# Optimization experiments

Hardware: AMD Instinct MI355X
Metric: run time of the kernel (lower is better)

Reference implementation:

```python
import jax, jax.numpy as jnp
from jax import lax
import numpy as np
from functools import partial

B, N, T, H, L = 16, 256, 4, 128, 2
VOCAB, OUT_VOCAB, MAX_STEPS = 1000, 1000, 15


def setup_inputs() -> dict:
    key = jax.random.key(0)
    ks = jax.random.split(key, 13)
    data = jax.random.randint(ks[0], (B, N, T), 0, VOCAB)
    true_branch_nodes = jax.random.randint(ks[1], (B, N), 0, N)
    false_branch_nodes = jax.random.randint(ks[2], (B, N), 0, N)
    exit_index = jax.random.randint(ks[3], (B,), 0, N)
    steps = jax.random.randint(ks[4], (B,), 1, MAX_STEPS + 1)
    s_in = 1.0 / np.sqrt(H)
    s_cat = 1.0 / np.sqrt(2 * L * H)
    embed = jax.random.uniform(ks[5], (VOCAB, H), jnp.float32, -0.1, 0.1)
    Wi = jax.random.normal(ks[6], (L, H, 4 * H), jnp.float32) * s_in
    Wh = jax.random.normal(ks[7], (L, H, 4 * H), jnp.float32) * s_in
    b_lstm = jnp.zeros((L, 4 * H), jnp.float32)
    Wb = jax.random.normal(ks[8], (2 * L * H, 2), jnp.float32) * s_cat
    bb = jax.random.normal(ks[9], (2,), jnp.float32) * 1e-6
    Wo = jax.random.normal(ks[10], (2 * L * H, OUT_VOCAB), jnp.float32) * s_cat
    bo = jax.random.normal(ks[11], (OUT_VOCAB,), jnp.float32) * 1e-6
    return dict(data=data, true_branch_nodes=true_branch_nodes,
                false_branch_nodes=false_branch_nodes, exit_index=exit_index,
                steps=steps, embed=embed, Wi=Wi, Wh=Wh, b_lstm=b_lstm,
                Wb=Wb, bb=bb, Wo=Wo, bo=bo)


def _lstm_step(Wi_l, Wh_l, b_l, c, h, x):
    # flax LSTMCell math: gates from input (no bias) + recurrent (bias)
    z = x @ Wi_l + h @ Wh_l + b_l  # [..., 4H]
    i, f, g, o = jnp.split(z, 4, axis=-1)
    c2 = jax.nn.sigmoid(f) * c + jax.nn.sigmoid(i) * jnp.tanh(g)
    h2 = jax.nn.sigmoid(o) * jnp.tanh(c2)
    return c2, h2


def _forward(data, true_branch_nodes, false_branch_nodes, exit_index, steps,
             embed, Wi, Wh, b_lstm, Wb, bb, Wo, bo):
    emb = embed[data]                       # [B, N, T, H]
    cs = jnp.zeros((L, B, N, H), embed.dtype)
    hs = jnp.zeros((L, B, N, H), embed.dtype)
    ip = jnp.zeros((B, N), embed.dtype).at[:, 0].set(1.0)
    b_idx = jnp.arange(B)

    seg_b = jax.vmap(partial(jax.ops.segment_sum, num_segments=N))        # [B,N,...] , [B,N]
    seg_lb = jax.vmap(seg_b, in_axes=(0, None))                           # [L,B,N,H]

    def execute(cs, hs):
        # run the stacked LSTM over the T statement tokens at every node
        def tok_step(carry, x_t):
            cs, hs = carry
            inp = x_t
            nc, nh = [], []
            for l in range(L):
                c2, h2 = _lstm_step(Wi[l], Wh[l], b_lstm[l], cs[l], hs[l], inp)
                nc.append(c2); nh.append(h2)
                inp = h2
            return (jnp.stack(nc), jnp.stack(nh)), None
        (cs, hs), _ = lax.scan(tok_step, (cs, hs), jnp.moveaxis(emb, 2, 0))
        return cs, hs

    def step(carry, _):
        cs, hs, ip, idx = carry
        cs_c, hs_c = execute(cs, hs)
        # exit node keeps its previous hidden state
        cs_c = cs_c.at[:, b_idx, exit_index].set(cs[:, b_idx, exit_index])
        hs_c = hs_c.at[:, b_idx, exit_index].set(hs[:, b_idx, exit_index])
        # branch decision from concatenated (c, h) of every layer: [B, N, 2LH]
        feats = jnp.concatenate([x for l in range(L) for x in (cs_c[l], hs_c[l])], axis=-1)
        branch = jax.nn.softmax(feats @ Wb + bb, axis=-1)
        wt = branch[..., 0] * ip            # [B, N]
        wf = branch[..., 1] * ip
        ip_new = seg_b(wt, true_branch_nodes) + seg_b(wf, false_branch_nodes)
        denom = (ip_new + 1e-7)[None, :, :, None]
        def agg(h):
            return (seg_lb(h * wt[None, :, :, None], true_branch_nodes)
                    + seg_lb(h * wf[None, :, :, None], false_branch_nodes)) / denom
        cs_new, hs_new = agg(cs_c), agg(hs_c)
        live = idx < steps                   # [B]
        cs = jnp.where(live[None, :, None, None], cs_new, cs)
        hs = jnp.where(live[None, :, None, None], hs_new, hs)
        ip = jnp.where(live[:, None], ip_new, ip)
        return (cs, hs, ip, idx + 1), None

    (cs, hs, ip, _), _ = lax.scan(step, (cs, hs, ip, jnp.zeros((), jnp.int32)),
                                  None, length=MAX_STEPS)
    fc = cs[:, b_idx, exit_index]           # [L, B, H]
    fh = hs[:, b_idx, exit_index]
    final = jnp.concatenate([x for l in range(L) for x in (fc[l], fh[l])], axis=-1)
    logits = final @ Wo + bo                # [B, OUT_VOCAB]
    return logits[:, None, :]


def reference(data, true_branch_nodes, false_branch_nodes, exit_index, steps,
              embed, Wi, Wh, b_lstm, Wb, bb, Wo, bo):
    return _forward(data, true_branch_nodes, false_branch_nodes, exit_index,
                    steps, embed, Wi, Wh, b_lstm, Wb, bb, Wo, bo)
```

## Files before the change

kernel.cpp:

```cpp
#include <hip/hip_runtime.h>
#include <hip/hip_bf16.h>
#include <stdint.h>
#include <stddef.h>

static constexpr int BB = 16, NN = 256, TT = 4, HH = 128;
static constexpr int MM = BB * NN;
static constexpr int CC = 512;
static constexpr int OUTV = 1000;
static constexpr int MAXS = 15;
static constexpr int SP = 132;

typedef float f32x4 __attribute__((ext_vector_type(4)));
typedef short s16x8 __attribute__((ext_vector_type(8)));

__device__ __forceinline__ float sigf(float x) { return 1.0f / (1.0f + __expf(-x)); }
__device__ __forceinline__ float tanhr(float x) { return 2.0f / (1.0f + __expf(-2.0f * x)) - 1.0f; }
__device__ __forceinline__ unsigned short f2bu(float a) {
  return __builtin_bit_cast(unsigned short, __float2bfloat16(a));
}


__global__ void init_kernel(float* __restrict__ S, float* __restrict__ ip, int* __restrict__ count) {
  int tid = blockIdx.x * blockDim.x + threadIdx.x;
  int stride = gridDim.x * blockDim.x;
  int total = 4 * MM * HH;
  for (int i = tid; i < total; i += stride) S[i] = 0.0f;
  for (int i = tid; i < MM; i += stride) {
    ip[i] = ((i & (NN - 1)) == 0) ? 1.0f : 0.0f;
    count[i] = 0;
  }
}

__global__ void swz_kernel(const float* __restrict__ W, unsigned short* __restrict__ out) {
  int i = blockIdx.x * 256 + threadIdx.x;
  int j = i & 7, ln = (i >> 3) & 63, kb = (i >> 9) & 3, ct = i >> 11;
  int n = ln & 15, q = ln >> 4;
  int k = kb * 32 + q * 8 + j;
  int col = ct * 16 + n;
  out[i] = f2bu(W[k * CC + col]);
}

__global__ void xw0tab_kernel(const float* __restrict__ embed, const float* __restrict__ Wi0,
                              const float* __restrict__ b0, float* __restrict__ tab) {
  const int v0 = blockIdx.x * 8;
  const int j = threadIdx.x;
  __shared__ float A[8][HH];
  for (int s = j; s < 8 * HH; s += 256) {
    int r = s >> 7, k = s & 127;
    int v = v0 + r; if (v >= OUTV) v = OUTV - 1;
    A[r][k] = embed[(size_t)v * HH + k];
  }
  __syncthreads();
  float za[8], zb[8];
  {
    float ba = b0[j], bbv = b0[j + 256];
#pragma unroll
    for (int r = 0; r < 8; ++r) { za[r] = ba; zb[r] = bbv; }
  }
#pragma unroll 4
  for (int k = 0; k < HH; ++k) {
    float wa = Wi0[k * CC + j], wb = Wi0[k * CC + j + 256];
#pragma unroll
    for (int r = 0; r < 8; ++r) { za[r] += A[r][k] * wa; zb[r] += A[r][k] * wb; }
  }
#pragma unroll
  for (int r = 0; r < 8; ++r) {
    tab[(size_t)(v0 + r) * CC + j] = za[r];
    tab[(size_t)(v0 + r) * CC + j + 256] = zb[r];
  }
}

__global__ void edge_count(const int* __restrict__ tb, const int* __restrict__ fb,
                           int* __restrict__ count) {
  int e = blockIdx.x * blockDim.x + threadIdx.x;
  if (e >= 2 * MM) return;
  int b = e >> 9, r = e & 511, n = r >> 1, bit = r & 1;
  int tgt = bit ? fb[b * NN + n] : tb[b * NN + n];
  atomicAdd(&count[b * NN + tgt], 1);
}

__global__ void edge_scan(int* __restrict__ count, int* __restrict__ offs) {
  int b = blockIdx.x, tid = threadIdx.x;
  __shared__ int s[256];
  int v = count[b * NN + tid];
  s[tid] = v;
  __syncthreads();
  for (int off = 1; off < 256; off <<= 1) {
    int t = (tid >= off) ? s[tid - off] : 0;
    __syncthreads();
    s[tid] += t;
    __syncthreads();
  }
  offs[b * NN + tid] = b * 2 * NN + s[tid] - v;
  count[b * NN + tid] = 0;
  if (b == 0 && tid == 0) offs[MM] = 2 * MM;
}

__global__ void edge_fill(const int* __restrict__ tb, const int* __restrict__ fb,
                          const int* __restrict__ offs, int* __restrict__ cursor,
                          int* __restrict__ edges) {
  int e = blockIdx.x * blockDim.x + threadIdx.x;
  if (e >= 2 * MM) return;
  int b = e >> 9, r = e & 511, n = r >> 1, bit = r & 1;
  int tgt = bit ? fb[b * NN + n] : tb[b * NN + n];
  int pos = offs[b * NN + tgt] + atomicAdd(&cursor[b * NN + tgt], 1);
  edges[pos] = (n << 1) | bit;
}


__global__ __launch_bounds__(512, 2) void step_kernel(
    float* __restrict__ Sc0g, float* __restrict__ Sh0g,
    float* __restrict__ Sc1g, float* __restrict__ Sh1g,
    const float* __restrict__ Wr0, const float* __restrict__ Wr1,
    const float* __restrict__ Wr2, const float* __restrict__ Wr3,
    float* __restrict__ Ww0, float* __restrict__ Ww1,
    float* __restrict__ Ww2, float* __restrict__ Ww3,
    const float* __restrict__ wtR, const float* __restrict__ wfR,
    float* __restrict__ wtW, float* __restrict__ wfW,
    const float* __restrict__ ipg,
    const int* __restrict__ offs, const int* __restrict__ edges,
    const float* __restrict__ tab,
    const unsigned short* __restrict__ swzWh0, const unsigned short* __restrict__ swzWi1,
    const unsigned short* __restrict__ swzWh1, const float* __restrict__ b1,
    const float* __restrict__ Wb, const float* __restrict__ bb,
    const int* __restrict__ data, const int* __restrict__ exi,
    const int* __restrict__ steps, int step) {
  const int row0 = blockIdx.x * 16;
  const int b = row0 >> 8;
  const int sb = steps[b];
  const bool aggLive = (step >= 1) && ((step - 1) < sb);
  const bool lstmLive = (step < sb);
  if (!aggLive && !lstmLive) return;

  const int tid = threadIdx.x;
  const int w = tid >> 6;
  const int lane = tid & 63;
  const int n16 = lane & 15, qq = lane >> 4;
  const int kcol = w * 16 + n16;

  __shared__ float c0L[16 * SP], h0L[16 * SP], c1L[16 * SP], h1L[16 * SP];
  __shared__ __align__(16) unsigned short hA0[2048], hA1[2048];
  __shared__ float exitP[4][HH];
  __shared__ float ipL[16];
  __shared__ int toks[64];

  if (aggLive) {
    const int l = tid & 31;
    const int m = tid >> 5;
    const int node = row0 + m;
    int beg = offs[node], end = offs[node + 1];
    float a0x = 0.f, a0y = 0.f, a0z = 0.f, a0w = 0.f;
    float a1x = 0.f, a1y = 0.f, a1z = 0.f, a1w = 0.f;
    float a2x = 0.f, a2y = 0.f, a2z = 0.f, a2w = 0.f;
    float a3x = 0.f, a3y = 0.f, a3z = 0.f, a3w = 0.f;
    float wsum = 0.f;
    for (int e = beg; e < end; ++e) {
      int rec = edges[e];
      int src = (b << 8) + (rec >> 1);
      float wv = (rec & 1) ? wfR[src] : wtR[src];
      wsum += wv;
      float4 x0 = ((const float4*)Wr0)[src * 32 + l];
      float4 x1 = ((const float4*)Wr1)[src * 32 + l];
      float4 x2 = ((const float4*)Wr2)[src * 32 + l];
      float4 x3 = ((const float4*)Wr3)[src * 32 + l];
      a0x += wv * x0.x; a0y += wv * x0.y; a0z += wv * x0.z; a0w += wv * x0.w;
      a1x += wv * x1.x; a1y += wv * x1.y; a1z += wv * x1.z; a1w += wv * x1.w;
      a2x += wv * x2.x; a2y += wv * x2.y; a2z += wv * x2.z; a2w += wv * x2.w;
      a3x += wv * x3.x; a3y += wv * x3.y; a3z += wv * x3.z; a3w += wv * x3.w;
    }
    float inv = 1.0f / (wsum + 1e-7f);
    float4 o0 = { a0x * inv, a0y * inv, a0z * inv, a0w * inv };
    float4 o1 = { a1x * inv, a1y * inv, a1z * inv, a1w * inv };
    float4 o2 = { a2x * inv, a2y * inv, a2z * inv, a2w * inv };
    float4 o3 = { a3x * inv, a3y * inv, a3z * inv, a3w * inv };
    ((float4*)c0L)[m * (SP / 4) + l] = o0;
    ((float4*)h0L)[m * (SP / 4) + l] = o1;
    ((float4*)c1L)[m * (SP / 4) + l] = o2;
    ((float4*)h1L)[m * (SP / 4) + l] = o3;
    if (l == 0) ipL[m] = wsum;
    if (!lstmLive) {
      ((float4*)Sc0g)[node * 32 + l] = o0;
      ((float4*)Sh0g)[node * 32 + l] = o1;
      ((float4*)Sc1g)[node * 32 + l] = o2;
      ((float4*)Sh1g)[node * 32 + l] = o3;
    }
  } else {
    for (int s = tid; s < 16 * HH; s += 512) {
      int m = s >> 7, k = s & 127;
      size_t g = (size_t)(row0 + m) * HH + k;
      c0L[m * SP + k] = Sc0g[g];
      h0L[m * SP + k] = Sh0g[g];
      c1L[m * SP + k] = Sc1g[g];
      h1L[m * SP + k] = Sh1g[g];
    }
    if (tid < 16) ipL[tid] = ipg[row0 + tid];
  }
  if (!lstmLive) return;

  s16x8 B0[4][4], B1[4][4];
  const s16x8* pWh0 = (const s16x8*)swzWh0;
  const s16x8* pWh1 = (const s16x8*)swzWh1;
  const s16x8* pWi1 = (const s16x8*)swzWi1;
  float b1v[4];
#pragma unroll
  for (int g = 0; g < 4; ++g) {
    int ci = w + 8 * g;
#pragma unroll
    for (int kb = 0; kb < 4; ++kb) {
      B0[g][kb] = pWh0[(ci * 4 + kb) * 64 + lane];
      B1[g][kb] = pWh1[(ci * 4 + kb) * 64 + lane];
    }
    b1v[g] = b1[ci * 16 + n16];
  }

  const int exnode = exi[b];
  const int exm = exnode - (row0 & (NN - 1));
  if (tid < 64) toks[tid] = data[(row0 + (tid >> 2)) * TT + (tid & 3)];
  __syncthreads();

  if (exm >= 0 && exm < 16 && tid < 128) {
    exitP[0][tid] = c0L[exm * SP + tid];
    exitP[1][tid] = h0L[exm * SP + tid];
    exitP[2][tid] = c1L[exm * SP + tid];
    exitP[3][tid] = h1L[exm * SP + tid];
  }

  const int kb0 = kcol >> 5, q0 = (kcol >> 3) & 3, j0 = kcol & 7;
  const int basePos = (kb0 * 64 + q0 * 16) * 8 + j0;
  float c0r[4], c1r[4], h0r[4], h1r[4];
#pragma unroll
  for (int r = 0; r < 4; ++r) {
    int m = qq * 4 + r;
    c0r[r] = c0L[m * SP + kcol];
    c1r[r] = c1L[m * SP + kcol];
    h0r[r] = h0L[m * SP + kcol];
    h1r[r] = h1L[m * SP + kcol];
    hA0[basePos + m * 8] = f2bu(h0r[r]);
    hA1[basePos + m * 8] = f2bu(h1r[r]);
  }
  __syncthreads();

  const s16x8* hA0v = (const s16x8*)hA0;
  const s16x8* hA1v = (const s16x8*)hA1;

  for (int t = 0; t < TT; ++t) {
    s16x8 a0[4], a1b[4];
#pragma unroll
    for (int kb = 0; kb < 4; ++kb) { a0[kb] = hA0v[kb * 64 + lane]; a1b[kb] = hA1v[kb * 64 + lane]; }
    f32x4 d0[4];
#pragma unroll
    for (int g = 0; g < 4; ++g) {
      int colz = (w + 8 * g) * 16 + n16;
#pragma unroll
      for (int r = 0; r < 4; ++r)
        d0[g][r] = tab[(size_t)toks[(qq * 4 + r) * 4 + t] * CC + colz];
    }
    __syncthreads();

#pragma unroll
    for (int g = 0; g < 4; ++g)
#pragma unroll
      for (int kb = 0; kb < 4; ++kb)
        d0[g] = __builtin_amdgcn_mfma_f32_16x16x32_bf16(a0[kb], B0[g][kb], d0[g], 0, 0, 0);

#pragma unroll
    for (int r = 0; r < 4; ++r) {
      float cn = sigf(d0[1][r]) * c0r[r] + sigf(d0[0][r]) * tanhr(d0[2][r]);
      float hn = sigf(d0[3][r]) * tanhr(cn);
      c0r[r] = cn; h0r[r] = hn;
      hA0[basePos + (qq * 4 + r) * 8] = f2bu(hn);
    }
    __syncthreads();

    s16x8 a1a[4];
#pragma unroll
    for (int kb = 0; kb < 4; ++kb) a1a[kb] = hA0v[kb * 64 + lane];
    f32x4 d1[4];
#pragma unroll
    for (int g = 0; g < 4; ++g) {
      int ci = w + 8 * g;
      s16x8 wi[4];
#pragma unroll
      for (int kb = 0; kb < 4; ++kb) wi[kb] = pWi1[(ci * 4 + kb) * 64 + lane];
      f32x4 d = { b1v[g], b1v[g], b1v[g], b1v[g] };
#pragma unroll
      for (int kb = 0; kb < 4; ++kb)
        d = __builtin_amdgcn_mfma_f32_16x16x32_bf16(a1a[kb], wi[kb], d, 0, 0, 0);
#pragma unroll
      for (int kb = 0; kb < 4; ++kb)
        d = __builtin_amdgcn_mfma_f32_16x16x32_bf16(a1b[kb], B1[g][kb], d, 0, 0, 0);
      d1[g] = d;
    }

#pragma unroll
    for (int r = 0; r < 4; ++r) {
      float cn = sigf(d1[1][r]) * c1r[r] + sigf(d1[0][r]) * tanhr(d1[2][r]);
      float hn = sigf(d1[3][r]) * tanhr(cn);
      c1r[r] = cn; h1r[r] = hn;
      hA1[basePos + (qq * 4 + r) * 8] = f2bu(hn);
    }
    __syncthreads();
  }

#pragma unroll
  for (int r = 0; r < 4; ++r) {
    int m = qq * 4 + r;
    c0L[m * SP + kcol] = c0r[r];
    h0L[m * SP + kcol] = h0r[r];
    c1L[m * SP + kcol] = c1r[r];
    h1L[m * SP + kcol] = h1r[r];
  }
  __syncthreads();

  {
    const int m = tid >> 5, sub = tid & 31;
    const int row = row0 + m;
    const bool isExit = (m == exm);
    float z0 = 0.f, z1 = 0.f;
#pragma unroll
    for (int u = 0; u < 16; ++u) {
      int k = u * 32 + sub;
      int seg = k >> 7, kk = k & 127;
      float fk;
      if (isExit) {
        fk = exitP[seg][kk];
      } else {
        fk = (seg == 0) ? c0L[m * SP + kk] : (seg == 1) ? h0L[m * SP + kk]
           : (seg == 2) ? c1L[m * SP + kk] : h1L[m * SP + kk];
      }
      z0 += fk * Wb[2 * k];
      z1 += fk * Wb[2 * k + 1];
    }
#pragma unroll
    for (int off = 16; off >= 1; off >>= 1) {
      z0 += __shfl_xor(z0, off);
      z1 += __shfl_xor(z1, off);
    }
    if (sub == 0) {
      z0 += bb[0]; z1 += bb[1];
      float mx = fmaxf(z0, z1);
      float e0 = __expf(z0 - mx), e1 = __expf(z1 - mx);
      float inv = 1.0f / (e0 + e1);
      float ipv = ipL[m];
      wtW[row] = e0 * inv * ipv;
      wfW[row] = e1 * inv * ipv;
    }
  }

  for (int s = tid; s < 16 * HH; s += 512) {
    int m = s >> 7, k = s & 127;
    bool ex = (m == exm);
    size_t g = (size_t)(row0 + m) * HH + k;
    Ww0[g] = ex ? exitP[0][k] : c0L[m * SP + k];
    Ww1[g] = ex ? exitP[1][k] : h0L[m * SP + k];
    Ww2[g] = ex ? exitP[2][k] : c1L[m * SP + k];
    Ww3[g] = ex ? exitP[3][k] : h1L[m * SP + k];
  }
}

__global__ void final_kernel(const float* __restrict__ Sc0, const float* __restrict__ Sh0,
                             const float* __restrict__ Sc1, const float* __restrict__ Sh1,
                             const int* __restrict__ exi, const float* __restrict__ Wo,
                             const float* __restrict__ bo, float* __restrict__ out) {
  const int b = blockIdx.x >> 2;
  const int vt = blockIdx.x & 3;
  const int tid = threadIdx.x;
  __shared__ float f[512];
  int row = b * NN + exi[b];
  if (tid < 128) {
    size_t g = (size_t)row * HH + tid;
    f[tid] = Sc0[g];
    f[128 + tid] = Sh0[g];
    f[256 + tid] = Sc1[g];
    f[384 + tid] = Sh1[g];
  }
  __syncthreads();
  if (tid < 250) {
    int v = vt * 250 + tid;
    float acc = bo[v];
#pragma unroll 8
    for (int k = 0; k < 512; ++k) acc += f[k] * Wo[(size_t)k * OUTV + v];
    out[b * OUTV + v] = acc;
  }
}

__global__ void zero_out_kernel(float* __restrict__ out, int n) {
  int i = blockIdx.x * blockDim.x + threadIdx.x;
  if (i < n) out[i] = 0.0f;
}


extern "C" void kernel_launch(void* const* d_in, const int* in_sizes, int n_in,
                              void* d_out, int out_size, void* d_ws, size_t ws_size,
                              hipStream_t stream) {
  const int* data = (const int*)d_in[0];
  const int* tb   = (const int*)d_in[1];
  const int* fb   = (const int*)d_in[2];
  const int* exi  = (const int*)d_in[3];
  const int* steps = (const int*)d_in[4];
  const float* embed = (const float*)d_in[5];
  const float* Wi = (const float*)d_in[6];
  const float* Wh = (const float*)d_in[7];
  const float* bl = (const float*)d_in[8];
  const float* Wb = (const float*)d_in[9];
  const float* bb = (const float*)d_in[10];
  const float* Wo = (const float*)d_in[11];
  const float* bo = (const float*)d_in[12];
  float* out = (float*)d_out;

  const float* Wi0 = Wi;
  const float* Wi1 = Wi + HH * CC;
  const float* Wh0 = Wh;
  const float* Wh1 = Wh + HH * CC;
  const float* b0 = bl;
  const float* b1 = bl + CC;

  float* ws = (float*)d_ws;
  size_t off = 0;
  float* tab = ws + off;  off += (size_t)1024 * CC;
  float* Sc0 = ws + off;  off += (size_t)MM * HH;
  float* Sh0 = ws + off;  off += (size_t)MM * HH;
  float* Sc1 = ws + off;  off += (size_t)MM * HH;
  float* Sh1 = ws + off;  off += (size_t)MM * HH;
  float* WA[4], *WB[4];
  for (int i = 0; i < 4; ++i) { WA[i] = ws + off; off += (size_t)MM * HH; }
  for (int i = 0; i < 4; ++i) { WB[i] = ws + off; off += (size_t)MM * HH; }
  unsigned short* swzWh0 = (unsigned short*)(ws + off); off += (size_t)HH * CC / 2;
  unsigned short* swzWi1 = (unsigned short*)(ws + off); off += (size_t)HH * CC / 2;
  unsigned short* swzWh1 = (unsigned short*)(ws + off); off += (size_t)HH * CC / 2;
  float* ip = ws + off;   off += MM;
  float* wtA = ws + off;  off += MM;
  float* wfA = ws + off;  off += MM;
  float* wtB = ws + off;  off += MM;
  float* wfB = ws + off;  off += MM;
  int* count = (int*)(ws + off); off += MM;
  int* offs  = (int*)(ws + off); off += MM + 16;
  int* edges = (int*)(ws + off); off += 2 * MM;
  (void)in_sizes; (void)n_in; (void)out_size;

  if (ws_size < off * sizeof(float)) {
    zero_out_kernel<<<(BB * OUTV + 255) / 256, 256, 0, stream>>>(out, BB * OUTV);
    return;
  }

  init_kernel<<<256, 256, 0, stream>>>(Sc0, ip, count);
  swz_kernel<<<256, 256, 0, stream>>>(Wh0, swzWh0);
  swz_kernel<<<256, 256, 0, stream>>>(Wi1, swzWi1);
  swz_kernel<<<256, 256, 0, stream>>>(Wh1, swzWh1);
  xw0tab_kernel<<<128, 256, 0, stream>>>(embed, Wi0, b0, tab);
  edge_count<<<(2 * MM + 255) / 256, 256, 0, stream>>>(tb, fb, count);
  edge_scan<<<BB, 256, 0, stream>>>(count, offs);
  edge_fill<<<(2 * MM + 255) / 256, 256, 0, stream>>>(tb, fb, offs, count, edges);

  for (int s = 0; s <= MAXS; ++s) {
    float** Wwr = (s & 1) ? WB : WA;
    float** Wrd = (s & 1) ? WA : WB;
    float* wtWp = (s & 1) ? wtB : wtA;
    float* wfWp = (s & 1) ? wfB : wfA;
    float* wtRp = (s & 1) ? wtA : wtB;
    float* wfRp = (s & 1) ? wfA : wfB;
    step_kernel<<<MM / 16, 512, 0, stream>>>(
        Sc0, Sh0, Sc1, Sh1,
        Wrd[0], Wrd[1], Wrd[2], Wrd[3],
        Wwr[0], Wwr[1], Wwr[2], Wwr[3],
        wtRp, wfRp, wtWp, wfWp, ip,
        offs, edges, tab, swzWh0, swzWi1, swzWh1, b1, Wb, bb,
        data, exi, steps, s);
  }
  final_kernel<<<BB * 4, 256, 0, stream>>>(Sc0, Sh0, Sc1, Sh1, exi, Wo, bo, out);
}
```

Baseline: 596.4 us.

## Fuse all setup, step and final kernels into one cooperative persistent kernel

Replaces the roughly 25 separate launches (init, swizzle, table build, edge CSR build, 16 step launches and the final projection) with one cooperative kernel of 256 blocks, using grid.sync between phases and steps. Loop-invariant bf16 weight fragments are loaded into registers once instead of every step. The state-zeroing init kernel and the full state arrays are dropped: zero state is synthesized in LDS and only the exit-node row is saved for the final projection. The aim is to remove launch overhead and redundant global traffic, at the cost of depending on all blocks being co-resident and on the expense of grid-wide barriers.

```diff
diff --git a/kernel.cpp b/kernel.cpp
--- a/kernel.cpp
+++ b/kernel.cpp
@@ -1,7 +1,10 @@
 #include <hip/hip_runtime.h>
+#include <hip/hip_cooperative_groups.h>
 #include <hip/hip_bf16.h>
 #include <stdint.h>
 #include <stddef.h>
+
+namespace cg = cooperative_groups;
 
 static constexpr int BB = 16, NN = 256, TT = 4, HH = 128;
 static constexpr int MM = BB * NN;
@@ -9,6 +12,7 @@
 static constexpr int OUTV = 1000;
 static constexpr int MAXS = 15;
 static constexpr int SP = 132;
+static constexpr int SSZ = MM * HH;
 
 typedef float f32x4 __attribute__((ext_vector_type(4)));
 typedef short s16x8 __attribute__((ext_vector_type(8)));
@@ -19,368 +23,336 @@
   return __builtin_bit_cast(unsigned short, __float2bfloat16(a));
 }
 
-
-__global__ void init_kernel(float* __restrict__ S, float* __restrict__ ip, int* __restrict__ count) {
-  int tid = blockIdx.x * blockDim.x + threadIdx.x;
-  int stride = gridDim.x * blockDim.x;
-  int total = 4 * MM * HH;
-  for (int i = tid; i < total; i += stride) S[i] = 0.0f;
-  for (int i = tid; i < MM; i += stride) {
-    ip[i] = ((i & (NN - 1)) == 0) ? 1.0f : 0.0f;
-    count[i] = 0;
-  }
-}
-
-__global__ void swz_kernel(const float* __restrict__ W, unsigned short* __restrict__ out) {
-  int i = blockIdx.x * 256 + threadIdx.x;
-  int j = i & 7, ln = (i >> 3) & 63, kb = (i >> 9) & 3, ct = i >> 11;
-  int n = ln & 15, q = ln >> 4;
-  int k = kb * 32 + q * 8 + j;
-  int col = ct * 16 + n;
-  out[i] = f2bu(W[k * CC + col]);
-}
-
-__global__ void xw0tab_kernel(const float* __restrict__ embed, const float* __restrict__ Wi0,
-                              const float* __restrict__ b0, float* __restrict__ tab) {
-  const int v0 = blockIdx.x * 8;
-  const int j = threadIdx.x;
-  __shared__ float A[8][HH];
-  for (int s = j; s < 8 * HH; s += 256) {
-    int r = s >> 7, k = s & 127;
-    int v = v0 + r; if (v >= OUTV) v = OUTV - 1;
-    A[r][k] = embed[(size_t)v * HH + k];
-  }
-  __syncthreads();
-  float za[8], zb[8];
-  {
-    float ba = b0[j], bbv = b0[j + 256];
-#pragma unroll
-    for (int r = 0; r < 8; ++r) { za[r] = ba; zb[r] = bbv; }
-  }
+__global__ __launch_bounds__(512, 2) void mega_kernel(
+    const int* __restrict__ data, const int* __restrict__ tb, const int* __restrict__ fb,
+    const int* __restrict__ exi, const int* __restrict__ steps,
+    const float* __restrict__ embed, const float* __restrict__ Wi, const float* __restrict__ Wh,
+    const float* __restrict__ bl, const float* __restrict__ Wb, const float* __restrict__ bbp,
+    const float* __restrict__ Wo, const float* __restrict__ bo,
+    float* __restrict__ out, float* __restrict__ ws) {
+  cg::grid_group grid = cg::this_grid();
+  const int blk = blockIdx.x;
+  const int tid = threadIdx.x;
+
+  float* tab = ws;
+  float* WAb = ws + (size_t)1024 * CC;
+  float* WBb = WAb + 4 * (size_t)SSZ;
+  unsigned short* swz = (unsigned short*)(WBb + 4 * (size_t)SSZ);
+  float* wtwf = (float*)(swz + 3 * 65536);
+  int* offs = (int*)(wtwf + 4 * MM);
+  int* edges = offs + MM + 16;
+  float* fin = (float*)(edges + 2 * MM);
+
+  const float* Wi0 = Wi;
+  const float* Wi1 = Wi + HH * CC;
+  const float* Wh0 = Wh;
+  const float* Wh1 = Wh + HH * CC;
+  const float* b0 = bl;
+  const float* b1 = bl + CC;
+  unsigned short* swzWh0 = swz;
+  unsigned short* swzWi1 = swz + 65536;
+  unsigned short* swzWh1 = swz + 2 * 65536;
+  float* wtA = wtwf;          float* wfA = wtwf + MM;
+  float* wtB = wtwf + 2 * MM; float* wfB = wtwf + 3 * MM;
+
+  __shared__ float c0L[16 * SP], h0L[16 * SP], c1L[16 * SP], h1L[16 * SP];
+  __shared__ __align__(16) unsigned short hA0[2048], hA1[2048];
+  __shared__ float exitP[512];
+  __shared__ float ipL[16];
+  __shared__ int toks[64];
+
+  for (int i = blk * 512 + tid; i < 3 * 65536; i += 256 * 512) {
+    int mtx = i >> 16, ii = i & 65535;
+    const float* W = (mtx == 0) ? Wh0 : (mtx == 1) ? Wi1 : Wh1;
+    int j = ii & 7, ln = (ii >> 3) & 63, kb = (ii >> 9) & 3, ct = ii >> 11;
+    int n = ln & 15, q = ln >> 4;
+    swz[i] = f2bu(W[(kb * 32 + q * 8 + j) * CC + ct * 16 + n]);
+  }
+  if (blk < 16) {
+    int* cnt = (int*)h0L;
+    int* sc = cnt + 256;
+    int* cur = cnt + 512;
+    if (tid < 256) cnt[tid] = 0;
+    __syncthreads();
+    const int n = tid >> 1, bit = tid & 1;
+    const int tgt = bit ? fb[blk * NN + n] : tb[blk * NN + n];
+    atomicAdd(&cnt[tgt], 1);
+    __syncthreads();
+    if (tid < 256) sc[tid] = cnt[tid];
+    __syncthreads();
+    for (int ofs = 1; ofs < 256; ofs <<= 1) {
+      int t2 = (tid < 256 && tid >= ofs) ? sc[tid - ofs] : 0;
+      __syncthreads();
+      if (tid < 256) sc[tid] += t2;
+      __syncthreads();
+    }
+    if (tid < 256) { offs[blk * NN + tid] = blk * 2 * NN + sc[tid] - cnt[tid]; cur[tid] = 0; }
+    if (blk == 0 && tid == 0) offs[MM] = 2 * MM;
+    __syncthreads();
+    int lpos = sc[tgt] - cnt[tgt] + atomicAdd(&cur[tgt], 1);
+    edges[blk * 2 * NN + lpos] = (n << 1) | bit;
+  }
+  if (blk < 250) {
+    float* A = c0L;
+    const int v0 = blk * 4;
+    A[tid] = embed[(size_t)(v0 + (tid >> 7)) * HH + (tid & 127)];
+    __syncthreads();
+    const int j = tid;
+    float a0 = b0[j], a1 = a0, a2 = a0, a3 = a0;
 #pragma unroll 4
-  for (int k = 0; k < HH; ++k) {
-    float wa = Wi0[k * CC + j], wb = Wi0[k * CC + j + 256];
-#pragma unroll
-    for (int r = 0; r < 8; ++r) { za[r] += A[r][k] * wa; zb[r] += A[r][k] * wb; }
-  }
-#pragma unroll
-  for (int r = 0; r < 8; ++r) {
-    tab[(size_t)(v0 + r) * CC + j] = za[r];
-    tab[(size_t)(v0 + r) * CC + j + 256] = zb[r];
-  }
-}
-
-__global__ void edge_count(const int* __restrict__ tb, const int* __restrict__ fb,
-                           int* __restrict__ count) {
-  int e = blockIdx.x * blockDim.x + threadIdx.x;
-  if (e >= 2 * MM) return;
-  int b = e >> 9, r = e & 511, n = r >> 1, bit = r & 1;
-  int tgt = bit ? fb[b * NN + n] : tb[b * NN + n];
-  atomicAdd(&count[b * NN + tgt], 1);
-}
-
-__global__ void edge_scan(int* __restrict__ count, int* __restrict__ offs) {
-  int b = blockIdx.x, tid = threadIdx.x;
-  __shared__ int s[256];
-  int v = count[b * NN + tid];
-  s[tid] = v;
-  __syncthreads();
-  for (int off = 1; off < 256; off <<= 1) {
-    int t = (tid >= off) ? s[tid - off] : 0;
-    __syncthreads();
-    s[tid] += t;
-    __syncthreads();
-  }
-  offs[b * NN + tid] = b * 2 * NN + s[tid] - v;
-  count[b * NN + tid] = 0;
-  if (b == 0 && tid == 0) offs[MM] = 2 * MM;
-}
-
-__global__ void edge_fill(const int* __restrict__ tb, const int* __restrict__ fb,
-                          const int* __restrict__ offs, int* __restrict__ cursor,
-                          int* __restrict__ edges) {
-  int e = blockIdx.x * blockDim.x + threadIdx.x;
-  if (e >= 2 * MM) return;
-  int b = e >> 9, r = e & 511, n = r >> 1, bit = r & 1;
-  int tgt = bit ? fb[b * NN + n] : tb[b * NN + n];
-  int pos = offs[b * NN + tgt] + atomicAdd(&cursor[b * NN + tgt], 1);
-  edges[pos] = (n << 1) | bit;
-}
-
-
-__global__ __launch_bounds__(512, 2) void step_kernel(
-    float* __restrict__ Sc0g, float* __restrict__ Sh0g,
-    float* __restrict__ Sc1g, float* __restrict__ Sh1g,
-    const float* __restrict__ Wr0, const float* __restrict__ Wr1,
-    const float* __restrict__ Wr2, const float* __restrict__ Wr3,
-    float* __restrict__ Ww0, float* __restrict__ Ww1,
-    float* __restrict__ Ww2, float* __restrict__ Ww3,
-    const float* __restrict__ wtR, const float* __restrict__ wfR,
-    float* __restrict__ wtW, float* __restrict__ wfW,
-    const float* __restrict__ ipg,
-    const int* __restrict__ offs, const int* __restrict__ edges,
-    const float* __restrict__ tab,
-    const unsigned short* __restrict__ swzWh0, const unsigned short* __restrict__ swzWi1,
-    const unsigned short* __restrict__ swzWh1, const float* __restrict__ b1,
-    const float* __restrict__ Wb, const float* __restrict__ bb,
-    const int* __restrict__ data, const int* __restrict__ exi,
-    const int* __restrict__ steps, int step) {
-  const int row0 = blockIdx.x * 16;
+    for (int k = 0; k < HH; ++k) {
+      float wv = Wi0[k * CC + j];
+      a0 += A[k] * wv; a1 += A[128 + k] * wv; a2 += A[256 + k] * wv; a3 += A[384 + k] * wv;
+    }
+    tab[(size_t)v0 * CC + j] = a0;
+    tab[(size_t)(v0 + 1) * CC + j] = a1;
+    tab[(size_t)(v0 + 2) * CC + j] = a2;
+    tab[(size_t)(v0 + 3) * CC + j] = a3;
+  }
+  if (tid < 64) toks[tid] = data[(blk * 16 + (tid >> 2)) * TT + (tid & 3)];
+
+  grid.sync();
+
+  const int row0 = blk * 16;
   const int b = row0 >> 8;
   const int sb = steps[b];
-  const bool aggLive = (step >= 1) && ((step - 1) < sb);
-  const bool lstmLive = (step < sb);
-  if (!aggLive && !lstmLive) return;
-
-  const int tid = threadIdx.x;
-  const int w = tid >> 6;
-  const int lane = tid & 63;
+  const int exnode = exi[b];
+  const int exm = exnode - (row0 & (NN - 1));
+  const int w = tid >> 6, lane = tid & 63;
   const int n16 = lane & 15, qq = lane >> 4;
   const int kcol = w * 16 + n16;
-
-  __shared__ float c0L[16 * SP], h0L[16 * SP], c1L[16 * SP], h1L[16 * SP];
-  __shared__ __align__(16) unsigned short hA0[2048], hA1[2048];
-  __shared__ float exitP[4][HH];
-  __shared__ float ipL[16];
-  __shared__ int toks[64];
-
-  if (aggLive) {
-    const int l = tid & 31;
-    const int m = tid >> 5;
-    const int node = row0 + m;
-    int beg = offs[node], end = offs[node + 1];
-    float a0x = 0.f, a0y = 0.f, a0z = 0.f, a0w = 0.f;
-    float a1x = 0.f, a1y = 0.f, a1z = 0.f, a1w = 0.f;
-    float a2x = 0.f, a2y = 0.f, a2z = 0.f, a2w = 0.f;
-    float a3x = 0.f, a3y = 0.f, a3z = 0.f, a3w = 0.f;
-    float wsum = 0.f;
-    for (int e = beg; e < end; ++e) {
-      int rec = edges[e];
-      int src = (b << 8) + (rec >> 1);
-      float wv = (rec & 1) ? wfR[src] : wtR[src];
-      wsum += wv;
-      float4 x0 = ((const float4*)Wr0)[src * 32 + l];
-      float4 x1 = ((const float4*)Wr1)[src * 32 + l];
-      float4 x2 = ((const float4*)Wr2)[src * 32 + l];
-      float4 x3 = ((const float4*)Wr3)[src * 32 + l];
-      a0x += wv * x0.x; a0y += wv * x0.y; a0z += wv * x0.z; a0w += wv * x0.w;
-      a1x += wv * x1.x; a1y += wv * x1.y; a1z += wv * x1.z; a1w += wv * x1.w;
-      a2x += wv * x2.x; a2y += wv * x2.y; a2z += wv * x2.z; a2w += wv * x2.w;
-      a3x += wv * x3.x; a3y += wv * x3.y; a3z += wv * x3.z; a3w += wv * x3.w;
-    }
-    float inv = 1.0f / (wsum + 1e-7f);
-    float4 o0 = { a0x * inv, a0y * inv, a0z * inv, a0w * inv };
-    float4 o1 = { a1x * inv, a1y * inv, a1z * inv, a1w * inv };
-    float4 o2 = { a2x * inv, a2y * inv, a2z * inv, a2w * inv };
-    float4 o3 = { a3x * inv, a3y * inv, a3z * inv, a3w * inv };
-    ((float4*)c0L)[m * (SP / 4) + l] = o0;
-    ((float4*)h0L)[m * (SP / 4) + l] = o1;
-    ((float4*)c1L)[m * (SP / 4) + l] = o2;
-    ((float4*)h1L)[m * (SP / 4) + l] = o3;
-    if (l == 0) ipL[m] = wsum;
-    if (!lstmLive) {
-      ((float4*)Sc0g)[node * 32 + l] = o0;
-      ((float4*)Sh0g)[node * 32 + l] = o1;
-      ((float4*)Sc1g)[node * 32 + l] = o2;
-      ((float4*)Sh1g)[node * 32 + l] = o3;
-    }
-  } else {
-    for (int s = tid; s < 16 * HH; s += 512) {
-      int m = s >> 7, k = s & 127;
-      size_t g = (size_t)(row0 + m) * HH + k;
-      c0L[m * SP + k] = Sc0g[g];
-      h0L[m * SP + k] = Sh0g[g];
-      c1L[m * SP + k] = Sc1g[g];
-      h1L[m * SP + k] = Sh1g[g];
-    }
-    if (tid < 16) ipL[tid] = ipg[row0 + tid];
-  }
-  if (!lstmLive) return;
-
-  s16x8 B0[4][4], B1[4][4];
+  const int basePos = ((kcol >> 5) * 64 + ((kcol >> 3) & 3) * 16) * 8 + (kcol & 7);
+
   const s16x8* pWh0 = (const s16x8*)swzWh0;
   const s16x8* pWh1 = (const s16x8*)swzWh1;
   const s16x8* pWi1 = (const s16x8*)swzWi1;
+  s16x8 B0f[4][4], B1f[4][4];
   float b1v[4];
 #pragma unroll
   for (int g = 0; g < 4; ++g) {
     int ci = w + 8 * g;
 #pragma unroll
     for (int kb = 0; kb < 4; ++kb) {
-      B0[g][kb] = pWh0[(ci * 4 + kb) * 64 + lane];
-      B1[g][kb] = pWh1[(ci * 4 + kb) * 64 + lane];
+      B0f[g][kb] = pWh0[(ci * 4 + kb) * 64 + lane];
+      B1f[g][kb] = pWh1[(ci * 4 + kb) * 64 + lane];
     }
     b1v[g] = b1[ci * 16 + n16];
   }
-
-  const int exnode = exi[b];
-  const int exm = exnode - (row0 & (NN - 1));
-  if (tid < 64) toks[tid] = data[(row0 + (tid >> 2)) * TT + (tid & 3)];
-  __syncthreads();
-
-  if (exm >= 0 && exm < 16 && tid < 128) {
-    exitP[0][tid] = c0L[exm * SP + tid];
-    exitP[1][tid] = h0L[exm * SP + tid];
-    exitP[2][tid] = c1L[exm * SP + tid];
-    exitP[3][tid] = h1L[exm * SP + tid];
-  }
-
-  const int kb0 = kcol >> 5, q0 = (kcol >> 3) & 3, j0 = kcol & 7;
-  const int basePos = (kb0 * 64 + q0 * 16) * 8 + j0;
-  float c0r[4], c1r[4], h0r[4], h1r[4];
-#pragma unroll
-  for (int r = 0; r < 4; ++r) {
-    int m = qq * 4 + r;
-    c0r[r] = c0L[m * SP + kcol];
-    c1r[r] = c1L[m * SP + kcol];
-    h0r[r] = h0L[m * SP + kcol];
-    h1r[r] = h1L[m * SP + kcol];
-    hA0[basePos + m * 8] = f2bu(h0r[r]);
-    hA1[basePos + m * 8] = f2bu(h1r[r]);
-  }
-  __syncthreads();
-
   const s16x8* hA0v = (const s16x8*)hA0;
   const s16x8* hA1v = (const s16x8*)hA1;
 
-  for (int t = 0; t < TT; ++t) {
-    s16x8 a0[4], a1b[4];
-#pragma unroll
-    for (int kb = 0; kb < 4; ++kb) { a0[kb] = hA0v[kb * 64 + lane]; a1b[kb] = hA1v[kb * 64 + lane]; }
-    f32x4 d0[4];
-#pragma unroll
-    for (int g = 0; g < 4; ++g) {
-      int colz = (w + 8 * g) * 16 + n16;
-#pragma unroll
-      for (int r = 0; r < 4; ++r)
-        d0[g][r] = tab[(size_t)toks[(qq * 4 + r) * 4 + t] * CC + colz];
-    }
-    __syncthreads();
-
-#pragma unroll
-    for (int g = 0; g < 4; ++g)
-#pragma unroll
-      for (int kb = 0; kb < 4; ++kb)
-        d0[g] = __builtin_amdgcn_mfma_f32_16x16x32_bf16(a0[kb], B0[g][kb], d0[g], 0, 0, 0);
-
+  for (int s = 0; s <= MAXS; ++s) {
+    if (s) grid.sync();
+    const bool aggLive = (s >= 1) && ((s - 1) < sb);
+    const bool lstmLive = s < sb;
+    if (!aggLive && !lstmLive) continue;
+
+    float* Ww0 = ((s & 1) ? WBb : WAb);             float* Ww1 = Ww0 + SSZ;
+    float* Ww2 = Ww0 + 2 * SSZ;                     float* Ww3 = Ww0 + 3 * SSZ;
+    const float* Wr0 = ((s & 1) ? WAb : WBb);       const float* Wr1 = Wr0 + SSZ;
+    const float* Wr2 = Wr0 + 2 * SSZ;               const float* Wr3 = Wr0 + 3 * SSZ;
+    float* wtWp = (s & 1) ? wtB : wtA;              float* wfWp = (s & 1) ? wfB : wfA;
+    const float* wtRp = (s & 1) ? wtA : wtB;        const float* wfRp = (s & 1) ? wfA : wfB;
+
+    if (aggLive) {
+      const int l = tid & 31;
+      const int m = tid >> 5;
+      const int node = row0 + m;
+      int beg = offs[node], end = offs[node + 1];
+      float a0x = 0.f, a0y = 0.f, a0z = 0.f, a0w = 0.f;
+      float a1x = 0.f, a1y = 0.f, a1z = 0.f, a1w = 0.f;
+      float a2x = 0.f, a2y = 0.f, a2z = 0.f, a2w = 0.f;
+      float a3x = 0.f, a3y = 0.f, a3z = 0.f, a3w = 0.f;
+      float wsum = 0.f;
+      for (int e = beg; e < end; ++e) {
+        int rec = edges[e];
+        int src = (b << 8) + (rec >> 1);
+        float wv = (rec & 1) ? wfRp[src] : wtRp[src];
+        wsum += wv;
+        float4 x0 = ((const float4*)Wr0)[src * 32 + l];
+        float4 x1 = ((const float4*)Wr1)[src * 32 + l];
+        float4 x2 = ((const float4*)Wr2)[src * 32 + l];
+        float4 x3 = ((const float4*)Wr3)[src * 32 + l];
+        a0x += wv * x0.x; a0y += wv * x0.y; a0z += wv * x0.z; a0w += wv * x0.w;
+        a1x += wv * x1.x; a1y += wv * x1.y; a1z += wv * x1.z; a1w += wv * x1.w;
+        a2x += wv * x2.x; a2y += wv * x2.y; a2z += wv * x2.z; a2w += wv * x2.w;
+        a3x += wv * x3.x; a3y += wv * x3.y; a3z += wv * x3.z; a3w += wv * x3.w;
+      }
+      float inv = 1.0f / (wsum + 1e-7f);
+      float4 o0 = { a0x * inv, a0y * inv, a0z * inv, a0w * inv };
+      float4 o1 = { a1x * inv, a1y * inv, a1z * inv, a1w * inv };
+      float4 o2 = { a2x * inv, a2y * inv, a2z * inv, a2w * inv };
+      float4 o3 = { a3x * inv, a3y * inv, a3z * inv, a3w * inv };
+      ((float4*)c0L)[m * (SP / 4) + l] = o0;
+      ((float4*)h0L)[m * (SP / 4) + l] = o1;
+      ((float4*)c1L)[m * (SP / 4) + l] = o2;
+      ((float4*)h1L)[m * (SP / 4) + l] = o3;
+      if (l == 0) ipL[m] = wsum;
+      if (!lstmLive && ((node & (NN - 1)) == exnode)) {
+        ((float4*)(fin + b * 512))[l] = o0;
+        ((float4*)(fin + b * 512 + 128))[l] = o1;
+        ((float4*)(fin + b * 512 + 256))[l] = o2;
+        ((float4*)(fin + b * 512 + 384))[l] = o3;
+      }
+    } else {
+      for (int i2 = tid; i2 < 16 * HH; i2 += 512) {
+        int m = i2 >> 7, k = i2 & 127;
+        c0L[m * SP + k] = 0.f; h0L[m * SP + k] = 0.f;
+        c1L[m * SP + k] = 0.f; h1L[m * SP + k] = 0.f;
+      }
+      if (tid < 16) ipL[tid] = (((row0 + tid) & (NN - 1)) == 0) ? 1.0f : 0.0f;
+    }
+    if (!lstmLive) continue;
+    __syncthreads();
+
+    if (exm >= 0 && exm < 16 && tid < 128) {
+      exitP[tid] = c0L[exm * SP + tid];
+      exitP[128 + tid] = h0L[exm * SP + tid];
+      exitP[256 + tid] = c1L[exm * SP + tid];
+      exitP[384 + tid] = h1L[exm * SP + tid];
+    }
+    float c0r[4], c1r[4], h0r[4], h1r[4];
 #pragma unroll
     for (int r = 0; r < 4; ++r) {
-      float cn = sigf(d0[1][r]) * c0r[r] + sigf(d0[0][r]) * tanhr(d0[2][r]);
-      float hn = sigf(d0[3][r]) * tanhr(cn);
-      c0r[r] = cn; h0r[r] = hn;
-      hA0[basePos + (qq * 4 + r) * 8] = f2bu(hn);
-    }
-    __syncthreads();
-
-    s16x8 a1a[4];
-#pragma unroll
-    for (int kb = 0; kb < 4; ++kb) a1a[kb] = hA0v[kb * 64 + lane];
-    f32x4 d1[4];
-#pragma unroll
-    for (int g = 0; g < 4; ++g) {
-      int ci = w + 8 * g;
-      s16x8 wi[4];
-#pragma unroll
-      for (int kb = 0; kb < 4; ++kb) wi[kb] = pWi1[(ci * 4 + kb) * 64 + lane];
-      f32x4 d = { b1v[g], b1v[g], b1v[g], b1v[g] };
-#pragma unroll
-      for (int kb = 0; kb < 4; ++kb)
-        d = __builtin_amdgcn_mfma_f32_16x16x32_bf16(a1a[kb], wi[kb], d, 0, 0, 0);
-#pragma unroll
-      for (int kb = 0; kb < 4; ++kb)
-        d = __builtin_amdgcn_mfma_f32_16x16x32_bf16(a1b[kb], B1[g][kb], d, 0, 0, 0);
-      d1[g] = d;
+      int m = qq * 4 + r;
+      c0r[r] = c0L[m * SP + kcol];
+      c1r[r] = c1L[m * SP + kcol];
+      h0r[r] = h0L[m * SP + kcol];
+      h1r[r] = h1L[m * SP + kcol];
+      hA0[basePos + m * 8] = f2bu(h0r[r]);
+      hA1[basePos + m * 8] = f2bu(h1r[r]);
+    }
+    __syncthreads();
+
+    for (int t = 0; t < TT; ++t) {
+      s16x8 a0[4], a1b[4];
+#pragma unroll
+      for (int kb = 0; kb < 4; ++kb) { a0[kb] = hA0v[kb * 64 + lane]; a1b[kb] = hA1v[kb * 64 + lane]; }
+      f32x4 d0[4];
+#pragma unroll
+      for (int g = 0; g < 4; ++g) {
+        int colz = (w + 8 * g) * 16 + n16;
+#pragma unroll
+        for (int r = 0; r < 4; ++r)
+          d0[g][r] = tab[(size_t)toks[(qq * 4 + r) * 4 + t] * CC + colz];
+      }
+      __syncthreads();
+
+#pragma unroll
+      for (int g = 0; g < 4; ++g)
+#pragma unroll
+        for (int kb = 0; kb < 4; ++kb)
+          d0[g] = __builtin_amdgcn_mfma_f32_16x16x32_bf16(a0[kb], B0f[g][kb], d0[g], 0, 0, 0);
+
+#pragma unroll
+      for (int r = 0; r < 4; ++r) {
+        float cn = sigf(d0[1][r]) * c0r[r] + sigf(d0[0][r]) * tanhr(d0[2][r]);
+        float hn = sigf(d0[3][r]) * tanhr(cn);
+        c0r[r] = cn; h0r[r] = hn;
+        hA0[basePos + (qq * 4 + r) * 8] = f2bu(hn);
+      }
+      __syncthreads();
+
+      s16x8 a1a[4];
+#pragma unroll
+      for (int kb = 0; kb < 4; ++kb) a1a[kb] = hA0v[kb * 64 + lane];
+      f32x4 d1[4];
+#pragma unroll
+      for (int g = 0; g < 4; ++g) {
+        int ci = w + 8 * g;
+        s16x8 wi[4];
+#pragma unroll
+        for (int kb = 0; kb < 4; ++kb) wi[kb] = pWi1[(ci * 4 + kb) * 64 + lane];
+        f32x4 d = { b1v[g], b1v[g], b1v[g], b1v[g] };
+#pragma unroll
+        for (int kb = 0; kb < 4; ++kb)
+          d = __builtin_amdgcn_mfma_f32_16x16x32_bf16(a1a[kb], wi[kb], d, 0, 0, 0);
+#pragma unroll
+        for (int kb = 0; kb < 4; ++kb)
+          d = __builtin_amdgcn_mfma_f32_16x16x32_bf16(a1b[kb], B1f[g][kb], d, 0, 0, 0);
+        d1[g] = d;
+      }
+
+#pragma unroll
+      for (int r = 0; r < 4; ++r) {
+        float cn = sigf(d1[1][r]) * c1r[r] + sigf(d1[0][r]) * tanhr(d1[2][r]);
+        float hn = sigf(d1[3][r]) * tanhr(cn);
+        c1r[r] = cn; h1r[r] = hn;
+        hA1[basePos + (qq * 4 + r) * 8] = f2bu(hn);
+      }
+      __syncthreads();
     }
 
 #pragma unroll
     for (int r = 0; r < 4; ++r) {
-      float cn = sigf(d1[1][r]) * c1r[r] + sigf(d1[0][r]) * tanhr(d1[2][r]);
-      float hn = sigf(d1[3][r]) * tanhr(cn);
-      c1r[r] = cn; h1r[r] = hn;
-      hA1[basePos + (qq * 4 + r) * 8] = f2bu(hn);
-    }
-    __syncthreads();
-  }
-
-#pragma unroll
-  for (int r = 0; r < 4; ++r) {
-    int m = qq * 4 + r;
-    c0L[m * SP + kcol] = c0r[r];
-    h0L[m * SP + kcol] = h0r[r];
-    c1L[m * SP + kcol] = c1r[r];
-    h1L[m * SP + kcol] = h1r[r];
-  }
-  __syncthreads();
-
-  {
-    const int m = tid >> 5, sub = tid & 31;
-    const int row = row0 + m;
-    const bool isExit = (m == exm);
-    float z0 = 0.f, z1 = 0.f;
-#pragma unroll
-    for (int u = 0; u < 16; ++u) {
-      int k = u * 32 + sub;
-      int seg = k >> 7, kk = k & 127;
-      float fk;
-      if (isExit) {
-        fk = exitP[seg][kk];
-      } else {
-        fk = (seg == 0) ? c0L[m * SP + kk] : (seg == 1) ? h0L[m * SP + kk]
-           : (seg == 2) ? c1L[m * SP + kk] : h1L[m * SP + kk];
-      }
-      z0 += fk * Wb[2 * k];
-      z1 += fk * Wb[2 * k + 1];
-    }
-#pragma unroll
-    for (int off = 16; off >= 1; off >>= 1) {
-      z0 += __shfl_xor(z0, off);
-      z1 += __shfl_xor(z1, off);
-    }
-    if (sub == 0) {
-      z0 += bb[0]; z1 += bb[1];
-      float mx = fmaxf(z0, z1);
-      float e0 = __expf(z0 - mx), e1 = __expf(z1 - mx);
-      float inv = 1.0f / (e0 + e1);
-      float ipv = ipL[m];
-      wtW[row] = e0 * inv * ipv;
-      wfW[row] = e1 * inv * ipv;
-    }
-  }
-
-  for (int s = tid; s < 16 * HH; s += 512) {
-    int m = s >> 7, k = s & 127;
-    bool ex = (m == exm);
-    size_t g = (size_t)(row0 + m) * HH + k;
-    Ww0[g] = ex ? exitP[0][k] : c0L[m * SP + k];
-    Ww1[g] = ex ? exitP[1][k] : h0L[m * SP + k];
-    Ww2[g] = ex ? exitP[2][k] : c1L[m * SP + k];
-    Ww3[g] = ex ? exitP[3][k] : h1L[m * SP + k];
-  }
-}
-
-__global__ void final_kernel(const float* __restrict__ Sc0, const float* __restrict__ Sh0,
-                             const float* __restrict__ Sc1, const float* __restrict__ Sh1,
-                             const int* __restrict__ exi, const float* __restrict__ Wo,
-                             const float* __restrict__ bo, float* __restrict__ out) {
-  const int b = blockIdx.x >> 2;
-  const int vt = blockIdx.x & 3;
-  const int tid = threadIdx.x;
-  __shared__ float f[512];
-  int row = b * NN + exi[b];
-  if (tid < 128) {
-    size_t g = (size_t)row * HH + tid;
-    f[tid] = Sc0[g];
-    f[128 + tid] = Sh0[g];
-    f[256 + tid] = Sc1[g];
-    f[384 + tid] = Sh1[g];
-  }
-  __syncthreads();
-  if (tid < 250) {
-    int v = vt * 250 + tid;
-    float acc = bo[v];
+      int m = qq * 4 + r;
+      c0L[m * SP + kcol] = c0r[r];
+      h0L[m * SP + kcol] = h0r[r];
+      c1L[m * SP + kcol] = c1r[r];
+      h1L[m * SP + kcol] = h1r[r];
+    }
+    __syncthreads();
+
+    {
+      const int m = tid >> 5, sub = tid & 31;
+      const int row = row0 + m;
+      const bool isExit = (m == exm);
+      float z0 = 0.f, z1 = 0.f;
+#pragma unroll
+      for (int u = 0; u < 16; ++u) {
+        int k = u * 32 + sub;
+        int seg = k >> 7, kk = k & 127;
+        float fk;
+        if (isExit) {
+          fk = exitP[seg * 128 + kk];
+        } else {
+          fk = (seg == 0) ? c0L[m * SP + kk] : (seg == 1) ? h0L[m * SP + kk]
+             : (seg == 2) ? c1L[m * SP + kk] : h1L[m * SP + kk];
+        }
+        z0 += fk * Wb[2 * k];
+        z1 += fk * Wb[2 * k + 1];
+      }
+#pragma unroll
+      for (int off = 16; off >= 1; off >>= 1) {
+        z0 += __shfl_xor(z0, off);
+        z1 += __shfl_xor(z1, off);
+      }
+      if (sub == 0) {
+        z0 += bbp[0]; z1 += bbp[1];
+        float mx = fmaxf(z0, z1);
+        float e0 = __expf(z0 - mx), e1 = __expf(z1 - mx);
+        float inv = 1.0f / (e0 + e1);
+        float ipv = ipL[m];
+        wtWp[row] = e0 * inv * ipv;
+        wfWp[row] = e1 * inv * ipv;
+      }
+    }
+
+    for (int s2 = tid; s2 < 16 * HH; s2 += 512) {
+      int m = s2 >> 7, k = s2 & 127;
+      bool ex = (m == exm);
+      size_t g = (size_t)(row0 + m) * HH + k;
+      Ww0[g] = ex ? exitP[k] : c0L[m * SP + k];
+      Ww1[g] = ex ? exitP[128 + k] : h0L[m * SP + k];
+      Ww2[g] = ex ? exitP[256 + k] : c1L[m * SP + k];
+      Ww3[g] = ex ? exitP[384 + k] : h1L[m * SP + k];
+    }
+  }
+
+  grid.sync();
+
+  if (blk < 32) {
+    const int fb2 = blk >> 1;
+    float* f = exitP;
+    f[tid] = fin[fb2 * 512 + tid];
+    __syncthreads();
+    int v = (blk & 1) * 512 + tid;
+    if (v < OUTV) {
+      float acc = bo[v];
 #pragma unroll 8
-    for (int k = 0; k < 512; ++k) acc += f[k] * Wo[(size_t)k * OUTV + v];
-    out[b * OUTV + v] = acc;
+      for (int k = 0; k < 512; ++k) acc += f[k] * Wo[(size_t)k * OUTV + v];
+      out[fb2 * OUTV + v] = acc;
+    }
   }
 }
 
@@ -403,69 +375,27 @@
   const float* Wh = (const float*)d_in[7];
   const float* bl = (const float*)d_in[8];
   const float* Wb = (const float*)d_in[9];
-  const float* bb = (const float*)d_in[10];
+  const float* bbp = (const float*)d_in[10];
   const float* Wo = (const float*)d_in[11];
   const float* bo = (const float*)d_in[12];
   float* out = (float*)d_out;
-
-  const float* Wi0 = Wi;
-  const float* Wi1 = Wi + HH * CC;
-  const float* Wh0 = Wh;
-  const float* Wh1 = Wh + HH * CC;
-  const float* b0 = bl;
-  const float* b1 = bl + CC;
-
   float* ws = (float*)d_ws;
-  size_t off = 0;
-  float* tab = ws + off;  off += (size_t)1024 * CC;
-  float* Sc0 = ws + off;  off += (size_t)MM * HH;
-  float* Sh0 = ws + off;  off += (size_t)MM * HH;
-  float* Sc1 = ws + off;  off += (size_t)MM * HH;
-  float* Sh1 = ws + off;  off += (size_t)MM * HH;
-  float* WA[4], *WB[4];
-  for (int i = 0; i < 4; ++i) { WA[i] = ws + off; off += (size_t)MM * HH; }
-  for (int i = 0; i < 4; ++i) { WB[i] = ws + off; off += (size_t)MM * HH; }
-  unsigned short* swzWh0 = (unsigned short*)(ws + off); off += (size_t)HH * CC / 2;
-  unsigned short* swzWi1 = (unsigned short*)(ws + off); off += (size_t)HH * CC / 2;
-  unsigned short* swzWh1 = (unsigned short*)(ws + off); off += (size_t)HH * CC / 2;
-  float* ip = ws + off;   off += MM;
-  float* wtA = ws + off;  off += MM;
-  float* wfA = ws + off;  off += MM;
-  float* wtB = ws + off;  off += MM;
-  float* wfB = ws + off;  off += MM;
-  int* count = (int*)(ws + off); off += MM;
-  int* offs  = (int*)(ws + off); off += MM + 16;
-  int* edges = (int*)(ws + off); off += 2 * MM;
   (void)in_sizes; (void)n_in; (void)out_size;
 
-  if (ws_size < off * sizeof(float)) {
+  size_t need = (size_t)1024 * CC
+              + 8 * (size_t)SSZ
+              + 3 * 32768
+              + 4 * MM
+              + (MM + 16) + 2 * MM
+              + 16 * 512;
+  if (ws_size < need * sizeof(float)) {
     zero_out_kernel<<<(BB * OUTV + 255) / 256, 256, 0, stream>>>(out, BB * OUTV);
     return;
   }
 
-  init_kernel<<<256, 256, 0, stream>>>(Sc0, ip, count);
-  swz_kernel<<<256, 256, 0, stream>>>(Wh0, swzWh0);
-  swz_kernel<<<256, 256, 0, stream>>>(Wi1, swzWi1);
-  swz_kernel<<<256, 256, 0, stream>>>(Wh1, swzWh1);
-  xw0tab_kernel<<<128, 256, 0, stream>>>(embed, Wi0, b0, tab);
-  edge_count<<<(2 * MM + 255) / 256, 256, 0, stream>>>(tb, fb, count);
-  edge_scan<<<BB, 256, 0, stream>>>(count, offs);
-  edge_fill<<<(2 * MM + 255) / 256, 256, 0, stream>>>(tb, fb, offs, count, edges);
-
-  for (int s = 0; s <= MAXS; ++s) {
-    float** Wwr = (s & 1) ? WB : WA;
-    float** Wrd = (s & 1) ? WA : WB;
-    float* wtWp = (s & 1) ? wtB : wtA;
-    float* wfWp = (s & 1) ? wfB : wfA;
-    float* wtRp = (s & 1) ? wtA : wtB;
-    float* wfRp = (s & 1) ? wfA : wfB;
-    step_kernel<<<MM / 16, 512, 0, stream>>>(
-        Sc0, Sh0, Sc1, Sh1,
-        Wrd[0], Wrd[1], Wrd[2], Wrd[3],
-        Wwr[0], Wwr[1], Wwr[2], Wwr[3],
-        wtRp, wfRp, wtWp, wfWp, ip,
-        offs, edges, tab, swzWh0, swzWi1, swzWh1, b1, Wb, bb,
-        data, exi, steps, s);
-  }
-  final_kernel<<<BB * 4, 256, 0, stream>>>(Sc0, Sh0, Sc1, Sh1, exi, Wo, bo, out);
+  void* kargs[] = { (void*)&data, (void*)&tb, (void*)&fb, (void*)&exi, (void*)&steps,
+                    (void*)&embed, (void*)&Wi, (void*)&Wh, (void*)&bl, (void*)&Wb,
+                    (void*)&bbp, (void*)&Wo, (void*)&bo, (void*)&out, (void*)&ws };
+  hipLaunchCooperativeKernel((const void*)mega_kernel, dim3(256), dim3(512),
+                             kargs, 0, stream);
 }
```

New measurement: 1.323 ms. 122% more time.
